# Kernel tuning notes

Hardware: AMD Instinct MI355X
Metric: run time of the kernel (lower is better)

## Reference

```python
import jax, jax.numpy as jnp
import numpy as np

B, T, D, H, E, O = 4, 2048, 512, 2048, 4, 512
C = 1024  # expert capacity
HE = H // E  # per-expert hidden width


def setup_inputs() -> dict:
    key = jax.random.key(0)
    ks = jax.random.split(key, 7)
    x = jax.random.normal(ks[0], (B, T, D), dtype=jnp.float32)
    dispatch_mask = jax.random.uniform(ks[1], (B, T, E, C), dtype=jnp.float32)
    combine_array = jax.random.uniform(ks[2], (B, T, E, C), dtype=jnp.float32)
    # per-expert parameters (fc1 contract, fc2 expand)
    w1 = jax.random.normal(ks[3], (E, D, HE), dtype=jnp.float32) * (1.0 / np.sqrt(D))
    b1 = jnp.zeros((E, HE), dtype=jnp.float32)
    w2 = jax.random.normal(ks[4], (E, HE, O), dtype=jnp.float32) * (1.0 / np.sqrt(HE))
    b2 = jnp.zeros((O,), dtype=jnp.float32)
    return {"x": x, "dispatch_mask": dispatch_mask, "combine_array": combine_array,
            "w1": w1, "b1": b1, "w2": w2, "b2": b2}


def reference(x, dispatch_mask, combine_array, w1, b1, w2, b2):
    # dispatch: gather tokens into per-expert capacity buffers [B,E,C,D]
    xd = jnp.einsum('btd,btec->becd', x, dispatch_mask)
    # per-expert fc1: [B,E,C,HE]
    h = jnp.einsum('becd,edh->bech', xd, w1) + b1[None, :, None, :]
    # GELU (exact erf form, matching torch nn.GELU default); norm/dropout are identity
    h = jax.nn.gelu(h, approximate=False)
    # per-expert fc2: [B,E,C,O]
    y = jnp.einsum('bech,eho->beco', h, w2)
    # combine: scatter expert outputs back to tokens [B,T,O]
    out = jnp.einsum('beco,btec->bto', y, combine_array) + b2
    return out
```

## Files before the change

### kernel.cpp

```cpp
#include <hip/hip_runtime.h>
#include <math.h>

namespace {

typedef short short8 __attribute__((ext_vector_type(8)));
typedef int i32x4 __attribute__((ext_vector_type(4)));
typedef float f32x4 __attribute__((ext_vector_type(4)));

constexpr int kB = 4, kT = 2048, kD = 512, kE = 4, kC = 1024, kHE = 512,
              kO = 512, kEC = 4096;

__device__ __forceinline__ unsigned short f2bf(float f) {
    unsigned int u = __float_as_uint(f);
    u += 0x7fffu + ((u >> 16) & 1u);
    return (unsigned short)(u >> 16);
}

__device__ __forceinline__ float gelu_exact(float v) {
    return 0.5f * v * (1.0f + erff(v * 0.70710678118654752f));
}

#define GLDS16(g, l)                                                      \
    __builtin_amdgcn_global_load_lds(                                     \
        (const __attribute__((address_space(1))) unsigned int*)(g),       \
        (__attribute__((address_space(3))) unsigned int*)(l), 16, 0, 0)

__global__ __launch_bounds__(256)
void transpose_cast(const float* __restrict__ in, unsigned short* __restrict__ out,
                    int R, int Cc, long long sIn, long long sOut)
{
    __shared__ float tile[32][33];
    const int z = blockIdx.z;
    const float* ip = in + (long long)z * sIn;
    unsigned short* op = out + (long long)z * sOut;
    const int c0 = blockIdx.x * 32, r0 = blockIdx.y * 32;
    const int tx = threadIdx.x & 31, ty = threadIdx.x >> 5;
#pragma unroll
    for (int i = 0; i < 4; ++i) {
        const int r = ty + i * 8;
        tile[r][tx] = ip[(size_t)(r0 + r) * Cc + c0 + tx];
    }
    __syncthreads();
#pragma unroll
    for (int i = 0; i < 4; ++i) {
        const int c = ty + i * 8;
        op[(size_t)(c0 + c) * R + r0 + tx] = f2bf(tile[tx][c]);
    }
}

__global__ __launch_bounds__(256)
void cast_bf16(const float* __restrict__ in, unsigned short* __restrict__ out,
               long long n)
{
    const long long i = ((long long)blockIdx.x * blockDim.x + threadIdx.x) * 4;
    if (i < n) {
        const float4 v = *(const float4*)&in[i];
        unsigned short o[4] = {f2bf(v.x), f2bf(v.y), f2bf(v.z), f2bf(v.w)};
        *(uint2*)&out[i] = *(const uint2*)o;
    }
}

template <int MODE>
__global__ __launch_bounds__(256, 1)
void mfma_gemm(const unsigned short* __restrict__ Aall,
               const unsigned short* __restrict__ Ball,
               const float* __restrict__ biasAll,
               void* __restrict__ Call,
               int M, int N, int K,
               long long sA, long long sB, long long sC,
               int zModA, int zModB, int zModBias, int biasStride, int bShift)
{
    __shared__ unsigned short As[4][128 * 64];
    __shared__ unsigned short Bs[4][128 * 64];

    const int z = blockIdx.z;
    const unsigned short* Ab = Aall + (long long)(z % zModA) * sA;
    const unsigned short* Bb = Ball + (long long)(z % zModB) * sB;
    const float* bias =
        (MODE != 0) ? biasAll + (long long)(z % zModBias) * biasStride : nullptr;

    const int gx = gridDim.x;
    int lin = blockIdx.y * gx + blockIdx.x;
    const int nwg = gx * gridDim.y;
    if ((nwg & 7) == 0) {
        const int q = nwg >> 3;
        lin = (lin & 7) * q + (lin >> 3);
    }
    const int gxs = 31 - __clz(gx);
    const int bx = lin & (gx - 1);
    const int by = lin >> gxs;
    const int row0 = by * 128;
    const int colB = bx * 128;

    const int t = threadIdx.x;
    const int lane = t & 63;
    const int w = t >> 6;
    const int wrow = w * 32;
    const int l8r = lane >> 3;
    const int l8c = ((lane & 7) ^ l8r) * 8;

    const int wm = (w >> 1) * 64;
    const int wn = (w & 1) * 64;
    const int fr = lane & 15;
    const int fq = (lane >> 4) * 8;
    const int fsw = (fr & 7) * 8;

    const unsigned int bMask = (1u << bShift) - 1u;

    f32x4 acc[4][4] = {};

    const unsigned aB0 =
        (unsigned)(size_t)(const __attribute__((address_space(3))) unsigned short*)
            &As[0][0] +
        (unsigned)(((wm + fr) * 64 + (fq ^ fsw)) * 2);
    const unsigned bB0 =
        (unsigned)(size_t)(const __attribute__((address_space(3))) unsigned short*)
            &Bs[0][0] +
        (unsigned)(((wn + fr) * 64 + (fq ^ fsw)) * 2);

    struct FragSet { i32x4 a0[4], a1[4], b0[4], b1[4]; };
    FragSet R0, R1;

#define DSR0(d, a) asm volatile("ds_read_b128 %0, %1" : "=v"(d) : "v"(a))
#define DSR1(d, a) asm volatile("ds_read_b128 %0, %1 offset:2048" : "=v"(d) : "v"(a))
#define DSR2(d, a) asm volatile("ds_read_b128 %0, %1 offset:4096" : "=v"(d) : "v"(a))
#define DSR3(d, a) asm volatile("ds_read_b128 %0, %1 offset:6144" : "=v"(d) : "v"(a))

#define READ16(R, CB)                                                         \
    do {                                                                      \
        const unsigned A0c = aB0 + (CB) * 16384u, A1c = A0c ^ 64u;            \
        const unsigned B0c = bB0 + (CB) * 16384u, B1c = B0c ^ 64u;            \
        DSR0(R.a0[0], A0c); DSR1(R.a0[1], A0c); DSR2(R.a0[2], A0c); DSR3(R.a0[3], A0c); \
        DSR0(R.b0[0], B0c); DSR1(R.b0[1], B0c); DSR2(R.b0[2], B0c); DSR3(R.b0[3], B0c); \
        DSR0(R.a1[0], A1c); DSR1(R.a1[1], A1c); DSR2(R.a1[2], A1c); DSR3(R.a1[3], A1c); \
        DSR0(R.b1[0], B1c); DSR1(R.b1[1], B1c); DSR2(R.b1[2], B1c); DSR3(R.b1[3], B1c); \
    } while (0)

#define MFMA16(R)                                                             \
    do {                                                                      \
        _Pragma("unroll") for (int i_ = 0; i_ < 4; ++i_)                      \
            _Pragma("unroll") for (int j_ = 0; j_ < 4; ++j_)                  \
                acc[i_][j_] = __builtin_amdgcn_mfma_f32_16x16x32_bf16(        \
                    __builtin_bit_cast(short8, R.a0[i_]),                     \
                    __builtin_bit_cast(short8, R.b0[j_]), acc[i_][j_], 0, 0, 0); \
        _Pragma("unroll") for (int i_ = 0; i_ < 4; ++i_)                      \
            _Pragma("unroll") for (int j_ = 0; j_ < 4; ++j_)                  \
                acc[i_][j_] = __builtin_amdgcn_mfma_f32_16x16x32_bf16(        \
                    __builtin_bit_cast(short8, R.a1[i_]),                     \
                    __builtin_bit_cast(short8, R.b1[j_]), acc[i_][j_], 0, 0, 0); \
    } while (0)

#define STAGE(buf, k0)                                                        \
    do {                                                                      \
        _Pragma("unroll")                                                     \
        for (int r = 0; r < 4; ++r) {                                         \
            const int ar = row0 + wrow + r * 8 + l8r;                         \
            GLDS16(Ab + (size_t)ar * K + ((k0) + l8c),                        \
                   &As[buf][(wrow + r * 8) * 64]);                            \
            const int bn = colB + wrow + r * 8 + l8r;                         \
            const int gk = (k0) + l8c;                                        \
            const size_t boff =                                               \
                (((size_t)(gk >> bShift) * N + bn) << bShift) + (gk & bMask); \
            GLDS16(Bb + boff, &Bs[buf][(wrow + r * 8) * 64]);                 \
        }                                                                     \
    } while (0)

#define ITER_FULL(T, CBRD, CBST, Rmf, Rrd)                                    \
    do {                                                                      \
        STAGE(CBST, ((T) + 2) * 64);                                          \
        asm volatile("s_waitcnt vmcnt(8)" ::: "memory");                      \
        __builtin_amdgcn_s_barrier();                                         \
        READ16(Rrd, CBRD);                                                    \
        MFMA16(Rmf);                                                          \
        asm volatile("s_waitcnt lgkmcnt(0)" ::: "memory");                    \
        __builtin_amdgcn_sched_barrier(0);                                    \
    } while (0)

    const int nt = K / 64;

    STAGE(0, 0);
    STAGE(1, 64);
    asm volatile("s_waitcnt vmcnt(8)" ::: "memory");
    __builtin_amdgcn_s_barrier();
    READ16(R0, 0);
    asm volatile("s_waitcnt lgkmcnt(0)" ::: "memory");
    __builtin_amdgcn_sched_barrier(0);

    for (int t0 = 0; t0 + 4 < nt; t0 += 4) {
        ITER_FULL(t0 + 0, 1, 2, R0, R1);
        ITER_FULL(t0 + 1, 2, 3, R1, R0);
        ITER_FULL(t0 + 2, 3, 0, R0, R1);
        ITER_FULL(t0 + 3, 0, 1, R1, R0);
    }
    ITER_FULL(nt - 4, 1, 2, R0, R1);
    ITER_FULL(nt - 3, 2, 3, R1, R0);
    asm volatile("s_waitcnt vmcnt(0)" ::: "memory");
    __builtin_amdgcn_s_barrier();
    READ16(R1, 3);
    MFMA16(R0);
    asm volatile("s_waitcnt lgkmcnt(0)" ::: "memory");
    __builtin_amdgcn_sched_barrier(0);
    MFMA16(R1);

#undef ITER_FULL
#undef STAGE
#undef MFMA16
#undef READ16
#undef DSR0
#undef DSR1
#undef DSR2
#undef DSR3

    const long long cz = (long long)z * sC;
#pragma unroll
    for (int i = 0; i < 4; ++i) {
        const int rowb = row0 + wm + i * 16 + (lane >> 4) * 4;
#pragma unroll
        for (int j = 0; j < 4; ++j) {
            const int col = colB + wn + j * 16 + fr;
            const float bv = (MODE != 0) ? bias[col] : 0.0f;
#pragma unroll
            for (int r = 0; r < 4; ++r) {
                const float v = acc[i][j][r];
                const size_t idx = (size_t)cz + (size_t)(rowb + r) * N + col;
                if (MODE == 0)
                    ((unsigned short*)Call)[idx] = f2bf(v);
                else if (MODE == 1)
                    ((unsigned short*)Call)[idx] = f2bf(gelu_exact(v + bv));
                else
                    ((float*)Call)[idx] = v + bv;
            }
        }
    }
}

}

extern "C" void kernel_launch(void* const* d_in, const int* in_sizes, int n_in,
                              void* d_out, int out_size, void* d_ws, size_t ws_size,
                              hipStream_t stream)
{
    const float* x    = (const float*)d_in[0];
    const float* mask = (const float*)d_in[1];
    const float* comb = (const float*)d_in[2];
    const float* w1   = (const float*)d_in[3];
    const float* b1   = (const float*)d_in[4];
    const float* w2   = (const float*)d_in[5];
    const float* b2   = (const float*)d_in[6];
    float* out = (float*)d_out;

    unsigned short* ws    = (unsigned short*)d_ws;
    unsigned short* regA  = ws;
    unsigned short* xT    = regA + 33554432;
    unsigned short* w1T   = xT + 4194304;
    unsigned short* w2T   = w1T + 1048576;
    unsigned short* xd    = w2T + 1048576;
    unsigned short* h     = xd + 8388608;
    unsigned short* maskT = regA;
    unsigned short* combB = regA;
    unsigned short* yT    = xd;

    dim3 blk(256);

    transpose_cast<<<dim3(kEC / 32, kT / 32, kB), blk, 0, stream>>>(
        mask, maskT, kT, kEC, (long long)kT * kEC, (long long)kT * kEC);
    transpose_cast<<<dim3(kD / 32, kT / 32, kB), blk, 0, stream>>>(
        x, xT, kT, kD, (long long)kT * kD, (long long)kT * kD);
    transpose_cast<<<dim3(kHE / 32, kD / 32, kE), blk, 0, stream>>>(
        w1, w1T, kD, kHE, (long long)kD * kHE, (long long)kD * kHE);
    transpose_cast<<<dim3(kO / 32, kHE / 32, kE), blk, 0, stream>>>(
        w2, w2T, kHE, kO, (long long)kHE * kO, (long long)kHE * kO);

    mfma_gemm<0><<<dim3(kD / 128, kEC / 128, kB), blk, 0, stream>>>(
        maskT, xT, nullptr, xd, kEC, kD, kT,
        (long long)kEC * kT, (long long)kD * kT, (long long)kEC * kD,
        kB, kB, 1, 0, 11);

    cast_bf16<<<dim3(33554432 / 4 / 256), blk, 0, stream>>>(
        comb, combB, 33554432LL);

    mfma_gemm<1><<<dim3(kHE / 128, kC / 128, kB * kE), blk, 0, stream>>>(
        xd, w1T, b1, h, kC, kHE, kD,
        (long long)kC * kD, (long long)kHE * kD, (long long)kC * kHE,
        kB * kE, kE, kE, kHE, 9);

    mfma_gemm<0><<<dim3(kC / 128, kO / 128, kB * kE), blk, 0, stream>>>(
        w2T, h, nullptr, yT, kO, kC, kHE,
        (long long)kO * kHE, (long long)kC * kHE, (long long)kO * kC,
        kE, kB * kE, 1, 0, 9);

    mfma_gemm<3><<<dim3(kO / 128, kT / 128, kB), blk, 0, stream>>>(
        combB, yT, b2, out, kT, kO, kEC,
        (long long)kT * kEC, (long long)kE * kO * kC, (long long)kT * kO,
        kB, kB, 1, 0, 10);
}
```

Measured before the change: 442.9 us.

## Fuse fp32 mask/combine conversion into GEMM A-operand loads

The dispatch and combine GEMMs now read the fp32 mask and combine arrays directly. They convert to bf16 in registers and write swizzled tiles into LDS, replacing the separate transpose_cast of the mask and the cast_bf16 pass over combine. This removes two full read-write passes over the two 128 MB tensors and shrinks the workspace. The price is register-staged, non-async A loads. For the mask the loads are strided scalar reads along the transposed axis, so coalescing may suffer. The remaining transpose_cast kernels now use 64-row tiles and packed 32-bit stores.

Measured after the change: 488.2 us. +10.2%, slower.

```diff
diff --git a/kernel.cpp b/kernel.cpp
--- a/kernel.cpp
+++ b/kernel.cpp
@@ -29,14 +29,14 @@
 void transpose_cast(const float* __restrict__ in, unsigned short* __restrict__ out,
                     int R, int Cc, long long sIn, long long sOut)
 {
-    __shared__ float tile[32][33];
+    __shared__ float tile[64][33];
     const int z = blockIdx.z;
     const float* ip = in + (long long)z * sIn;
     unsigned short* op = out + (long long)z * sOut;
-    const int c0 = blockIdx.x * 32, r0 = blockIdx.y * 32;
+    const int c0 = blockIdx.x * 32, r0 = blockIdx.y * 64;
     const int tx = threadIdx.x & 31, ty = threadIdx.x >> 5;
 #pragma unroll
-    for (int i = 0; i < 4; ++i) {
+    for (int i = 0; i < 8; ++i) {
         const int r = ty + i * 8;
         tile[r][tx] = ip[(size_t)(r0 + r) * Cc + c0 + tx];
     }
@@ -44,25 +44,15 @@
 #pragma unroll
     for (int i = 0; i < 4; ++i) {
         const int c = ty + i * 8;
-        op[(size_t)(c0 + c) * R + r0 + tx] = f2bf(tile[tx][c]);
-    }
-}
-
-__global__ __launch_bounds__(256)
-void cast_bf16(const float* __restrict__ in, unsigned short* __restrict__ out,
-               long long n)
-{
-    const long long i = ((long long)blockIdx.x * blockDim.x + threadIdx.x) * 4;
-    if (i < n) {
-        const float4 v = *(const float4*)&in[i];
-        unsigned short o[4] = {f2bf(v.x), f2bf(v.y), f2bf(v.z), f2bf(v.w)};
-        *(uint2*)&out[i] = *(const uint2*)o;
-    }
-}
-
-template <int MODE>
+        const unsigned lo = f2bf(tile[tx * 2][c]);
+        const unsigned hi = f2bf(tile[tx * 2 + 1][c]);
+        *(unsigned*)&op[(size_t)(c0 + c) * R + r0 + tx * 2] = lo | (hi << 16);
+    }
+}
+
+template <int MODE, int ASRC>
 __global__ __launch_bounds__(256, 1)
-void mfma_gemm(const unsigned short* __restrict__ Aall,
+void mfma_gemm(const void* __restrict__ AallV,
                const unsigned short* __restrict__ Ball,
                const float* __restrict__ biasAll,
                void* __restrict__ Call,
@@ -74,7 +64,12 @@
     __shared__ unsigned short Bs[4][128 * 64];
 
     const int z = blockIdx.z;
-    const unsigned short* Ab = Aall + (long long)(z % zModA) * sA;
+    const unsigned short* Ab =
+        (ASRC == 0) ? (const unsigned short*)AallV + (long long)(z % zModA) * sA
+                    : nullptr;
+    const float* Af =
+        (ASRC != 0) ? (const float*)AallV + (long long)(z % zModA) * sA
+                    : nullptr;
     const unsigned short* Bb = Ball + (long long)(z % zModB) * sB;
     const float* bias =
         (MODE != 0) ? biasAll + (long long)(z % zModBias) * biasStride : nullptr;
@@ -108,6 +103,16 @@
     const unsigned int bMask = (1u << bShift) - 1u;
 
     f32x4 acc[4][4] = {};
+
+    float ar[8][4];
+    const int a1_m = t & 15;
+    const int a1_k = (t >> 4) * 4;
+    const int a2_m = t >> 4;
+    const int a2_k = (t & 15) * 4;
+    const int aw_eoff =
+        (ASRC == 1)
+            ? (a1_m * 64 + (((a1_k >> 3) ^ (a1_m & 7)) << 3) + (a1_k & 7))
+            : (a2_m * 64 + (((a2_k >> 3) ^ (a2_m & 7)) << 3) + (a2_k & 7));
 
     const unsigned aB0 =
         (unsigned)(size_t)(const __attribute__((address_space(3))) unsigned short*)
@@ -150,13 +155,10 @@
                     __builtin_bit_cast(short8, R.b1[j_]), acc[i_][j_], 0, 0, 0); \
     } while (0)
 
-#define STAGE(buf, k0)                                                        \
+#define STAGE_B(buf, k0)                                                      \
     do {                                                                      \
         _Pragma("unroll")                                                     \
         for (int r = 0; r < 4; ++r) {                                         \
-            const int ar = row0 + wrow + r * 8 + l8r;                         \
-            GLDS16(Ab + (size_t)ar * K + ((k0) + l8c),                        \
-                   &As[buf][(wrow + r * 8) * 64]);                            \
             const int bn = colB + wrow + r * 8 + l8r;                         \
             const int gk = (k0) + l8c;                                        \
             const size_t boff =                                               \
@@ -165,9 +167,56 @@
         }                                                                     \
     } while (0)
 
-#define ITER_FULL(T, CBRD, CBST, Rmf, Rrd)                                    \
-    do {                                                                      \
-        STAGE(CBST, ((T) + 2) * 64);                                          \
+#define STAGE_A_GLDS(buf, k0)                                                 \
+    do {                                                                      \
+        _Pragma("unroll")                                                     \
+        for (int r = 0; r < 4; ++r) {                                         \
+            const int arow = row0 + wrow + r * 8 + l8r;                       \
+            GLDS16(Ab + (size_t)arow * K + ((k0) + l8c),                      \
+                   &As[buf][(wrow + r * 8) * 64]);                            \
+        }                                                                     \
+    } while (0)
+
+#define A_ISSUE(k0)                                                           \
+    do {                                                                      \
+        if constexpr (ASRC == 1) {                                            \
+            _Pragma("unroll")                                                 \
+            for (int p_ = 0; p_ < 8; ++p_) {                                  \
+                const size_t b_ =                                             \
+                    (size_t)((k0) + a1_k) * M + row0 + p_ * 16 + a1_m;        \
+                ar[p_][0] = Af[b_];                                           \
+                ar[p_][1] = Af[b_ + (size_t)M];                               \
+                ar[p_][2] = Af[b_ + 2 * (size_t)M];                           \
+                ar[p_][3] = Af[b_ + 3 * (size_t)M];                           \
+            }                                                                 \
+        } else {                                                              \
+            _Pragma("unroll")                                                 \
+            for (int p_ = 0; p_ < 8; ++p_) {                                  \
+                const float4 v_ = *(const float4*)&Af[                        \
+                    (size_t)(row0 + p_ * 16 + a2_m) * K + (k0) + a2_k];       \
+                ar[p_][0] = v_.x; ar[p_][1] = v_.y;                           \
+                ar[p_][2] = v_.z; ar[p_][3] = v_.w;                           \
+            }                                                                 \
+        }                                                                     \
+    } while (0)
+
+#define A_WRITE(buf)                                                          \
+    do {                                                                      \
+        _Pragma("unroll")                                                     \
+        for (int p_ = 0; p_ < 8; ++p_) {                                      \
+            unsigned lo_, hi_;                                                \
+            asm("v_cvt_pk_bf16_f32 %0, %1, %2"                                \
+                : "=v"(lo_) : "v"(ar[p_][0]), "v"(ar[p_][1]));                \
+            asm("v_cvt_pk_bf16_f32 %0, %1, %2"                                \
+                : "=v"(hi_) : "v"(ar[p_][2]), "v"(ar[p_][3]));                \
+            *(uint2*)&As[buf][aw_eoff + p_ * 1024] = make_uint2(lo_, hi_);    \
+        }                                                                     \
+    } while (0)
+
+#define ITER_BF16(T, CBRD, CBST, Rmf, Rrd)                                    \
+    do {                                                                      \
+        STAGE_A_GLDS(CBST, ((T) + 2) * 64);                                   \
+        STAGE_B(CBST, ((T) + 2) * 64);                                        \
         asm volatile("s_waitcnt vmcnt(8)" ::: "memory");                      \
         __builtin_amdgcn_s_barrier();                                         \
         READ16(Rrd, CBRD);                                                    \
@@ -176,34 +225,93 @@
         __builtin_amdgcn_sched_barrier(0);                                    \
     } while (0)
 
+#define ITER_F32(T, CBRD, CBST, Rmf, Rrd)                                     \
+    do {                                                                      \
+        A_ISSUE(((T) + 2) * 64);                                              \
+        STAGE_B(CBST, ((T) + 2) * 64);                                        \
+        if constexpr (ASRC == 1)                                              \
+            asm volatile("s_waitcnt vmcnt(36)" ::: "memory");                 \
+        else                                                                  \
+            asm volatile("s_waitcnt vmcnt(12)" ::: "memory");                 \
+        __builtin_amdgcn_sched_barrier(0);                                    \
+        __builtin_amdgcn_s_barrier();                                         \
+        READ16(Rrd, CBRD);                                                    \
+        MFMA16(Rmf);                                                          \
+        asm volatile("s_waitcnt vmcnt(4)" ::: "memory");                      \
+        __builtin_amdgcn_sched_barrier(0);                                    \
+        A_WRITE(CBST);                                                        \
+        asm volatile("s_waitcnt lgkmcnt(0)" ::: "memory");                    \
+        __builtin_amdgcn_sched_barrier(0);                                    \
+    } while (0)
+
     const int nt = K / 64;
 
-    STAGE(0, 0);
-    STAGE(1, 64);
-    asm volatile("s_waitcnt vmcnt(8)" ::: "memory");
-    __builtin_amdgcn_s_barrier();
-    READ16(R0, 0);
-    asm volatile("s_waitcnt lgkmcnt(0)" ::: "memory");
-    __builtin_amdgcn_sched_barrier(0);
-
-    for (int t0 = 0; t0 + 4 < nt; t0 += 4) {
-        ITER_FULL(t0 + 0, 1, 2, R0, R1);
-        ITER_FULL(t0 + 1, 2, 3, R1, R0);
-        ITER_FULL(t0 + 2, 3, 0, R0, R1);
-        ITER_FULL(t0 + 3, 0, 1, R1, R0);
-    }
-    ITER_FULL(nt - 4, 1, 2, R0, R1);
-    ITER_FULL(nt - 3, 2, 3, R1, R0);
-    asm volatile("s_waitcnt vmcnt(0)" ::: "memory");
-    __builtin_amdgcn_s_barrier();
-    READ16(R1, 3);
-    MFMA16(R0);
-    asm volatile("s_waitcnt lgkmcnt(0)" ::: "memory");
-    __builtin_amdgcn_sched_barrier(0);
-    MFMA16(R1);
-
-#undef ITER_FULL
-#undef STAGE
+    if constexpr (ASRC == 0) {
+        STAGE_A_GLDS(0, 0); STAGE_B(0, 0);
+        STAGE_A_GLDS(1, 64); STAGE_B(1, 64);
+        asm volatile("s_waitcnt vmcnt(8)" ::: "memory");
+        __builtin_amdgcn_s_barrier();
+        READ16(R0, 0);
+        asm volatile("s_waitcnt lgkmcnt(0)" ::: "memory");
+        __builtin_amdgcn_sched_barrier(0);
+
+        for (int t0 = 0; t0 + 4 < nt; t0 += 4) {
+            ITER_BF16(t0 + 0, 1, 2, R0, R1);
+            ITER_BF16(t0 + 1, 2, 3, R1, R0);
+            ITER_BF16(t0 + 2, 3, 0, R0, R1);
+            ITER_BF16(t0 + 3, 0, 1, R1, R0);
+        }
+        ITER_BF16(nt - 4, 1, 2, R0, R1);
+        ITER_BF16(nt - 3, 2, 3, R1, R0);
+        asm volatile("s_waitcnt vmcnt(0)" ::: "memory");
+        __builtin_amdgcn_s_barrier();
+        READ16(R1, 3);
+        MFMA16(R0);
+        asm volatile("s_waitcnt lgkmcnt(0)" ::: "memory");
+        __builtin_amdgcn_sched_barrier(0);
+        MFMA16(R1);
+    } else {
+        A_ISSUE(0);
+        asm volatile("s_waitcnt vmcnt(0)" ::: "memory");
+        __builtin_amdgcn_sched_barrier(0);
+        A_WRITE(0);
+        A_ISSUE(64);
+        STAGE_B(0, 0);
+        STAGE_B(1, 64);
+        asm volatile("s_waitcnt vmcnt(8)" ::: "memory");
+        __builtin_amdgcn_sched_barrier(0);
+        A_WRITE(1);
+        asm volatile("s_waitcnt lgkmcnt(0)" ::: "memory");
+        asm volatile("s_waitcnt vmcnt(4)" ::: "memory");
+        __builtin_amdgcn_sched_barrier(0);
+        __builtin_amdgcn_s_barrier();
+        READ16(R0, 0);
+        asm volatile("s_waitcnt lgkmcnt(0)" ::: "memory");
+        __builtin_amdgcn_sched_barrier(0);
+
+        for (int t0 = 0; t0 + 4 < nt; t0 += 4) {
+            ITER_F32(t0 + 0, 1, 2, R0, R1);
+            ITER_F32(t0 + 1, 2, 3, R1, R0);
+            ITER_F32(t0 + 2, 3, 0, R0, R1);
+            ITER_F32(t0 + 3, 0, 1, R1, R0);
+        }
+        ITER_F32(nt - 4, 1, 2, R0, R1);
+        ITER_F32(nt - 3, 2, 3, R1, R0);
+        asm volatile("s_waitcnt vmcnt(0)" ::: "memory");
+        __builtin_amdgcn_s_barrier();
+        READ16(R1, 3);
+        MFMA16(R0);
+        asm volatile("s_waitcnt lgkmcnt(0)" ::: "memory");
+        __builtin_amdgcn_sched_barrier(0);
+        MFMA16(R1);
+    }
+
+#undef ITER_F32
+#undef ITER_BF16
+#undef A_WRITE
+#undef A_ISSUE
+#undef STAGE_A_GLDS
+#undef STAGE_B
 #undef MFMA16
 #undef READ16
 #undef DSR0
@@ -249,48 +357,40 @@
     const float* b2   = (const float*)d_in[6];
     float* out = (float*)d_out;
 
-    unsigned short* ws    = (unsigned short*)d_ws;
-    unsigned short* regA  = ws;
-    unsigned short* xT    = regA + 33554432;
-    unsigned short* w1T   = xT + 4194304;
-    unsigned short* w2T   = w1T + 1048576;
-    unsigned short* xd    = w2T + 1048576;
-    unsigned short* h     = xd + 8388608;
-    unsigned short* maskT = regA;
-    unsigned short* combB = regA;
-    unsigned short* yT    = xd;
+    unsigned short* ws  = (unsigned short*)d_ws;
+    unsigned short* xT  = ws;
+    unsigned short* w1T = xT + 4194304;
+    unsigned short* w2T = w1T + 1048576;
+    unsigned short* xd  = w2T + 1048576;
+    unsigned short* h   = xd + 8388608;
+    unsigned short* yT  = xd;
 
     dim3 blk(256);
 
-    transpose_cast<<<dim3(kEC / 32, kT / 32, kB), blk, 0, stream>>>(
-        mask, maskT, kT, kEC, (long long)kT * kEC, (long long)kT * kEC);
-    transpose_cast<<<dim3(kD / 32, kT / 32, kB), blk, 0, stream>>>(
+    transpose_cast<<<dim3(kD / 32, kT / 64, kB), blk, 0, stream>>>(
         x, xT, kT, kD, (long long)kT * kD, (long long)kT * kD);
-    transpose_cast<<<dim3(kHE / 32, kD / 32, kE), blk, 0, stream>>>(
+    transpose_cast<<<dim3(kHE / 32, kD / 64, kE), blk, 0, stream>>>(
         w1, w1T, kD, kHE, (long long)kD * kHE, (long long)kD * kHE);
-    transpose_cast<<<dim3(kO / 32, kHE / 32, kE), blk, 0, stream>>>(
+    transpose_cast<<<dim3(kO / 32, kHE / 64, kE), blk, 0, stream>>>(
         w2, w2T, kHE, kO, (long long)kHE * kO, (long long)kHE * kO);
 
-    mfma_gemm<0><<<dim3(kD / 128, kEC / 128, kB), blk, 0, stream>>>(
-        maskT, xT, nullptr, xd, kEC, kD, kT,
+    mfma_gemm<0, 1><<<dim3(kD / 128, kEC / 128, kB), blk, 0, stream>>>(
+        mask, xT, nullptr, xd, kEC, kD, kT,
         (long long)kEC * kT, (long long)kD * kT, (long long)kEC * kD,
         kB, kB, 1, 0, 11);
 
-    cast_bf16<<<dim3(33554432 / 4 / 256), blk, 0, stream>>>(
-        comb, combB, 33554432LL);
-
-    mfma_gemm<1><<<dim3(kHE / 128, kC / 128, kB * kE), blk, 0, stream>>>(
+    mfma_gemm<1, 0><<<dim3(kHE / 128, kC / 128, kB * kE), blk, 0, stream>>>(
         xd, w1T, b1, h, kC, kHE, kD,
         (long long)kC * kD, (long long)kHE * kD, (long long)kC * kHE,
         kB * kE, kE, kE, kHE, 9);
 
-    mfma_gemm<0><<<dim3(kC / 128, kO / 128, kB * kE), blk, 0, stream>>>(
+    mfma_gemm<0, 0><<<dim3(kC / 128, kO / 128, kB * kE), blk, 0, stream>>>(
         w2T, h, nullptr, yT, kO, kC, kHE,
         (long long)kO * kHE, (long long)kC * kHE, (long long)kO * kC,
         kE, kB * kE, 1, 0, 9);
 
-    mfma_gemm<3><<<dim3(kO / 128, kT / 128, kB), blk, 0, stream>>>(
-        combB, yT, b2, out, kT, kO, kEC,
+    mfma_gemm<3, 2><<<dim3(kO / 128, kT / 128, kB), blk, 0, stream>>>(
+        comb, yT, b2, out, kT, kO, kEC,
         (long long)kT * kEC, (long long)kE * kO * kC, (long long)kT * kO,
         kB, kB, 1, 0, 10);
 }
```
